# Kernel tuning notes

Measured on AMD Instinct MI355X. Metric: run time of the kernel, lower is better.

Reference implementation:

```python
import jax, jax.numpy as jnp
import numpy as np

D_MODEL = 1024
N_HEADS = 16
HEAD_DIM = D_MODEL // N_HEADS
D_FF = 4096
B, S = 2, 2048
EPS = 1e-6
NEG = -1e9


def setup_inputs() -> dict:
    key = jax.random.key(0)
    ks = jax.random.split(key, 16)
    sd = 1.0 / np.sqrt(D_MODEL)
    sf = 1.0 / np.sqrt(D_FF)
    inp = {
        "x": jax.random.normal(ks[0], (B, S, D_MODEL), jnp.float32),
        # causal mask, broadcastable over batch and heads
        "mask": jnp.tril(jnp.ones((S, S), jnp.bool_))[None, None, :, :],
        # attention projections, torch Linear layout [out, in]
        "Wq": jax.random.normal(ks[1], (D_MODEL, D_MODEL), jnp.float32) * sd,
        "bq": jnp.zeros((D_MODEL,), jnp.float32),
        "Wk": jax.random.normal(ks[2], (D_MODEL, D_MODEL), jnp.float32) * sd,
        "bk": jnp.zeros((D_MODEL,), jnp.float32),
        "Wv": jax.random.normal(ks[3], (D_MODEL, D_MODEL), jnp.float32) * sd,
        "bv": jnp.zeros((D_MODEL,), jnp.float32),
        "Wo": jax.random.normal(ks[4], (D_MODEL, D_MODEL), jnp.float32) * sd,
        "bo": jnp.zeros((D_MODEL,), jnp.float32),
        # layer norms
        "ln1_g": jnp.ones((D_MODEL,), jnp.float32),
        "ln1_b": jnp.zeros((D_MODEL,), jnp.float32),
        "ln2_g": jnp.ones((D_MODEL,), jnp.float32),
        "ln2_b": jnp.zeros((D_MODEL,), jnp.float32),
        # FFN
        "W1": jax.random.normal(ks[5], (D_FF, D_MODEL), jnp.float32) * sd,
        "b1": jnp.zeros((D_FF,), jnp.float32),
        "W2": jax.random.normal(ks[6], (D_MODEL, D_FF), jnp.float32) * sf,
        "b2": jnp.zeros((D_MODEL,), jnp.float32),
    }
    return inp


def _layer_norm(x, g, b):
    mu = jnp.mean(x, axis=-1, keepdims=True)
    var = jnp.var(x, axis=-1, keepdims=True)
    return (x - mu) * jax.lax.rsqrt(var + EPS) * g + b


def _linear(x, W, b):
    return jnp.einsum('...i,oi->...o', x, W) + b


def _attention(x, mask, Wq, bq, Wk, bk, Wv, bv, Wo, bo):
    Bsz, Sq, _ = x.shape
    q = _linear(x, Wq, bq).reshape(Bsz, Sq, N_HEADS, HEAD_DIM)
    k = _linear(x, Wk, bk).reshape(Bsz, Sq, N_HEADS, HEAD_DIM)
    v = _linear(x, Wv, bv).reshape(Bsz, Sq, N_HEADS, HEAD_DIM)
    # [B,H,S,S]
    scores = jnp.einsum('bqhd,bkhd->bhqk', q, k) / np.sqrt(HEAD_DIM)
    scores = jnp.where(mask, scores, NEG)
    weights = jax.nn.softmax(scores, axis=-1)
    ctx = jnp.einsum('bhqk,bkhd->bqhd', weights, v).reshape(Bsz, Sq, D_MODEL)
    return _linear(ctx, Wo, bo)


def reference(x, mask, Wq, bq, Wk, bk, Wv, bv, Wo, bo,
              ln1_g, ln1_b, ln2_g, ln2_b, W1, b1, W2, b2):
    # pre-LN attention block (dropout = identity at inference)
    h = _layer_norm(x, ln1_g, ln1_b)
    x = x + _attention(h, mask, Wq, bq, Wk, bk, Wv, bv, Wo, bo)
    # pre-LN FFN block
    h = _layer_norm(x, ln2_g, ln2_b)
    h = jax.nn.gelu(_linear(h, W1, b1), approximate=False)
    x = x + _linear(h, W2, b2)
    return x
```

## Files before the change

kernel.cpp:

```cpp
#include <hip/hip_runtime.h>
#include <hip/hip_bf16.h>
#include <cstdint>
#include <cstddef>

typedef unsigned short u16;
typedef __bf16 bf16x8 __attribute__((ext_vector_type(8)));
typedef float f32x4 __attribute__((ext_vector_type(4)));

#define D_MODEL 1024
#define D_FF    4096
#define BATCH   2
#define SEQ     2048
#define NH      16
#define HD      64
#define ROWS    (BATCH*SEQ)
#define QKVS    3072

__device__ __forceinline__ u16 f2bf(float f) {
    union { float f; uint32_t u; } v; v.f = f;
    uint32_t u = v.u;
    u += 0x7FFF + ((u >> 16) & 1);
    return (u16)(u >> 16);
}

__device__ __forceinline__ uint32_t cvtpk_bf16(float lo, float hi) {
    uint32_t r;
    asm("v_cvt_pk_bf16_f32 %0, %1, %2" : "=v"(r) : "v"(lo), "v"(hi));
    return r;
}

__device__ __forceinline__ bf16x8 ldg8(const u16* p) {
    return *reinterpret_cast<const bf16x8*>(p);
}

__device__ __forceinline__ f32x4 mfma16(bf16x8 a, bf16x8 b, f32x4 c) {
    return __builtin_amdgcn_mfma_f32_16x16x32_bf16(a, b, c, 0, 0, 0);
}

__device__ __forceinline__ void gld_lds16(const void* g, void* l) {
    __builtin_amdgcn_global_load_lds(
        (const __attribute__((address_space(1))) void*)g,
        (__attribute__((address_space(3))) void*)l, 16, 0, 0);
}

struct alignas(8) U16x4 { u16 x, y, z, w; };

__global__ void cvt_all(const float* __restrict__ s0, const float* __restrict__ s1,
                        const float* __restrict__ s2, const float* __restrict__ s3,
                        const float* __restrict__ s4, const float* __restrict__ s5,
                        u16* __restrict__ out)
{
    const size_t MM1 = 1 << 20;
    size_t i = ((size_t)blockIdx.x * 256 + threadIdx.x) * 4;
    const float* src; size_t off;
    if      (i <     MM1) { src = s0; off = i; }
    else if (i < 2 * MM1) { src = s1; off = i - MM1; }
    else if (i < 3 * MM1) { src = s2; off = i - 2 * MM1; }
    else if (i < 4 * MM1) { src = s3; off = i - 3 * MM1; }
    else if (i < 8 * MM1) { src = s4; off = i - 4 * MM1; }
    else                  { src = s5; off = i - 8 * MM1; }
    float4 f = *reinterpret_cast<const float4*>(src + off);
    U16x4 o{ f2bf(f.x), f2bf(f.y), f2bf(f.z), f2bf(f.w) };
    *reinterpret_cast<U16x4*>(out + i) = o;
}

__global__ __launch_bounds__(256) void ln_bf16(
    const float* __restrict__ x, const float* __restrict__ g,
    const float* __restrict__ b, u16* __restrict__ out)
{
    int row = blockIdx.x;
    const float* xr = x + (size_t)row * D_MODEL;
    int t = threadIdx.x;
    float4 v = *reinterpret_cast<const float4*>(xr + t * 4);
    float s = v.x + v.y + v.z + v.w;
    float q = v.x*v.x + v.y*v.y + v.z*v.z + v.w*v.w;
    #pragma unroll
    for (int off = 1; off < 64; off <<= 1) {
        s += __shfl_xor(s, off);
        q += __shfl_xor(q, off);
    }
    __shared__ float red[8];
    if ((t & 63) == 0) { red[(t >> 6) * 2] = s; red[(t >> 6) * 2 + 1] = q; }
    __syncthreads();
    float sum = red[0] + red[2] + red[4] + red[6];
    float sq  = red[1] + red[3] + red[5] + red[7];
    float mu  = sum * (1.0f / D_MODEL);
    float var = sq * (1.0f / D_MODEL) - mu * mu;
    float rstd = rsqrtf(var + 1e-6f);
    float4 gg = *reinterpret_cast<const float4*>(g + t * 4);
    float4 bb = *reinterpret_cast<const float4*>(b + t * 4);
    U16x4 o{ f2bf((v.x - mu) * rstd * gg.x + bb.x),
             f2bf((v.y - mu) * rstd * gg.y + bb.y),
             f2bf((v.z - mu) * rstd * gg.z + bb.z),
             f2bf((v.w - mu) * rstd * gg.w + bb.w) };
    *reinterpret_cast<U16x4*>(out + (size_t)row * D_MODEL + t * 4) = o;
}

#define EPI_BF16   0
#define EPI_RESF32 1
#define EPI_GELU   2
#define EPI_PART   3

template<int EPI>
__global__ __launch_bounds__(512, 1) void gemm256(
    const u16* __restrict__ A, const u16* __restrict__ B,
    const float* __restrict__ bias, const float* __restrict__ res,
    u16* __restrict__ outb, float* __restrict__ outf,
    int M, int N, int K)
{
    __shared__ u16 As[2][256 * 64];
    __shared__ u16 Bs[2][256 * 64];
    const int t = threadIdx.x;
    const int lane = t & 63, w = t >> 6;
    const int lr = lane & 15, lg = lane >> 4;
    const int wr = w >> 2, wc = w & 3;

    const int gw  = N >> 8;
    const int nwg = gridDim.x;
    const int cpx = nwg >> 3;
    const int swz = ((int)blockIdx.x & 7) * cpx + ((int)blockIdx.x >> 3);
    const int by = swz / gw, bx = swz % gw;
    const int brow = by * 256, bcol = bx * 256;

    const u16* Ag = A + (size_t)brow * K;
    const u16* Bg = B + (size_t)bcol * K;

    f32x4 acc[8][4] = {};
    const int NT = K >> 6;

    auto stageAll = [&](int buf, int kt) {
        #pragma unroll
        for (int c = 0; c < 8; ++c) {
            const u16* g = (c < 4) ? Ag : Bg;
            u16* l = (c < 4) ? As[buf] : Bs[buf];
            int cc = c & 3;
            int row = cc * 64 + (t >> 3);
            int sg = (t & 7) ^ (row & 7);
            gld_lds16(g + (size_t)row * K + kt * 64 + sg * 8, l + cc * 4096 + t * 8);
        }
    };

    bf16x8 areg[4][2], breg[2][2][2];

    auto loadA = [&](const u16* la, int qm) {
        #pragma unroll
        for (int f = 0; f < 4; ++f) {
            int row = wr * 128 + qm * 64 + f * 16 + lr;
            const u16* bp = la + row * 64;
            int key = row & 7;
            areg[f][0] = ldg8(bp + ((0 + lg) ^ key) * 8);
            areg[f][1] = ldg8(bp + ((4 + lg) ^ key) * 8);
        }
    };
    auto loadB = [&](const u16* lb, int qn) {
        #pragma unroll
        for (int f = 0; f < 2; ++f) {
            int row = wc * 64 + qn * 32 + f * 16 + lr;
            const u16* bp = lb + row * 64;
            int key = row & 7;
            breg[qn][f][0] = ldg8(bp + ((0 + lg) ^ key) * 8);
            breg[qn][f][1] = ldg8(bp + ((4 + lg) ^ key) * 8);
        }
    };
    auto mmaQ = [&](int qm, int qn) {
        __builtin_amdgcn_s_setprio(1);
        #pragma unroll
        for (int mi = 0; mi < 4; ++mi) {
            #pragma unroll
            for (int fn = 0; fn < 2; ++fn) {
                acc[qm * 4 + mi][qn * 2 + fn] =
                    mfma16(areg[mi][0], breg[qn][fn][0], acc[qm * 4 + mi][qn * 2 + fn]);
                acc[qm * 4 + mi][qn * 2 + fn] =
                    mfma16(areg[mi][1], breg[qn][fn][1], acc[qm * 4 + mi][qn * 2 + fn]);
            }
        }
        __builtin_amdgcn_s_setprio(0);
    };

    stageAll(0, 0);
    stageAll(1, 1);
    asm volatile("s_waitcnt vmcnt(8)" ::: "memory");
    __builtin_amdgcn_s_barrier();

    for (int kt = 0; kt < NT; ++kt) {
        const int cur = kt & 1;
        const u16* la = As[cur];
        const u16* lb = Bs[cur];
        loadA(la, 0); loadB(lb, 0);
        __builtin_amdgcn_s_barrier();
        mmaQ(0, 0);
        __builtin_amdgcn_s_barrier();
        loadB(lb, 1);
        __builtin_amdgcn_s_barrier();
        mmaQ(0, 1);
        __builtin_amdgcn_s_barrier();
        loadA(la, 1);
        __builtin_amdgcn_s_barrier();
        mmaQ(1, 0);
        __builtin_amdgcn_s_barrier();
        mmaQ(1, 1);
        if (kt + 1 == NT) break;
        __builtin_amdgcn_s_barrier();
        if (kt + 2 < NT) {
            stageAll(cur, kt + 2);
            asm volatile("s_waitcnt vmcnt(8)" ::: "memory");
        } else {
            asm volatile("s_waitcnt vmcnt(0)" ::: "memory");
        }
        __builtin_amdgcn_s_barrier();
    }

    #pragma unroll
    for (int mi = 0; mi < 8; ++mi) {
        int r0 = brow + wr * 128 + mi * 16 + lg * 4;
        #pragma unroll
        for (int ni = 0; ni < 4; ++ni) {
            int c = bcol + wc * 64 + ni * 16 + lr;
            float bv = bias[c];
            #pragma unroll
            for (int j = 0; j < 4; ++j) {
                float v = acc[mi][ni][j] + bv;
                size_t idx = (size_t)(r0 + j) * N + c;
                if constexpr (EPI == EPI_GELU) {
                    v = 0.5f * v * (1.0f + erff(v * 0.70710678118f));
                    outb[idx] = f2bf(v);
                } else if constexpr (EPI == EPI_RESF32) {
                    outf[idx] = v + res[idx];
                } else {
                    outb[idx] = f2bf(v);
                }
            }
        }
    }
}

template<int EPI>
__global__ __launch_bounds__(256, 2) void gemm_bt(
    const u16* __restrict__ A, const u16* __restrict__ B,
    const float* __restrict__ bias, const float* __restrict__ res,
    u16* __restrict__ outb, float* __restrict__ outf,
    int M, int N, int K, int KS)
{
    __shared__ u16 As[2][128 * 64];
    __shared__ u16 Bs[2][128 * 64];
    const int t = threadIdx.x;
    const int lane = t & 63;
    const int w = t >> 6;
    const int lr = lane & 15, lg = lane >> 4;
    const int wrr = (w >> 1) * 64, wcc = (w & 1) * 64;
    const int brow = blockIdx.y * 128, bcol = blockIdx.x * 128;
    const int kz = blockIdx.z;
    const u16* Ag = A + (size_t)brow * KS + (size_t)kz * K;
    const u16* Bg = B + (size_t)bcol * KS + (size_t)kz * K;

    f32x4 acc[4][4] = {};

    const int NT = K >> 6;

    auto stage = [&](int buf, int kt) {
        const u16* ga = Ag + kt * 64;
        const u16* gb = Bg + kt * 64;
        u16* la = As[buf];
        u16* lb = Bs[buf];
        #pragma unroll
        for (int c = 0; c < 4; ++c) {
            int f = c * 256 + t;
            int row = f >> 3, slot = f & 7;
            int sg = slot ^ (row & 7);
            gld_lds16(ga + (size_t)row * KS + sg * 8, la + f * 8);
            gld_lds16(gb + (size_t)row * KS + sg * 8, lb + f * 8);
        }
    };

    auto compute = [&](int buf) {
        const u16* la = As[buf];
        const u16* lb = Bs[buf];
        bf16x8 af[4][2];
        #pragma unroll
        for (int mi = 0; mi < 4; ++mi) {
            int row = wrr + mi * 16 + lr;
            int base = row * 64;
            af[mi][0] = *reinterpret_cast<const bf16x8*>(la + base + ((0 + lg) ^ (row & 7)) * 8);
            af[mi][1] = *reinterpret_cast<const bf16x8*>(la + base + ((4 + lg) ^ (row & 7)) * 8);
        }
        __builtin_amdgcn_s_setprio(1);
        #pragma unroll
        for (int ni = 0; ni < 4; ++ni) {
            int row = wcc + ni * 16 + lr;
            int base = row * 64;
            bf16x8 b0 = *reinterpret_cast<const bf16x8*>(lb + base + ((0 + lg) ^ (row & 7)) * 8);
            bf16x8 b1 = *reinterpret_cast<const bf16x8*>(lb + base + ((4 + lg) ^ (row & 7)) * 8);
            #pragma unroll
            for (int mi = 0; mi < 4; ++mi) {
                acc[mi][ni] = mfma16(af[mi][0], b0, acc[mi][ni]);
                acc[mi][ni] = mfma16(af[mi][1], b1, acc[mi][ni]);
            }
        }
        __builtin_amdgcn_s_setprio(0);
    };

    stage(0, 0);
    if (NT > 1) {
        stage(1, 1);
        asm volatile("s_waitcnt vmcnt(8)" ::: "memory");
    } else {
        asm volatile("s_waitcnt vmcnt(0)" ::: "memory");
    }
    __builtin_amdgcn_s_barrier();

    for (int kt = 0; kt < NT; ++kt) {
        compute(kt & 1);
        if (kt + 1 == NT) break;
        __builtin_amdgcn_s_barrier();
        if (kt + 2 < NT) {
            stage(kt & 1, kt + 2);
            asm volatile("s_waitcnt vmcnt(8)" ::: "memory");
        } else {
            asm volatile("s_waitcnt vmcnt(0)" ::: "memory");
        }
        __builtin_amdgcn_s_barrier();
    }

    #pragma unroll
    for (int mi = 0; mi < 4; ++mi) {
        int r0 = brow + wrr + mi * 16 + lg * 4;
        #pragma unroll
        for (int ni = 0; ni < 4; ++ni) {
            int c = bcol + wcc + ni * 16 + lr;
            float bv = 0.f;
            if constexpr (EPI != EPI_PART) bv = bias[c];
            #pragma unroll
            for (int j = 0; j < 4; ++j) {
                float v = acc[mi][ni][j] + bv;
                size_t idx = (size_t)(r0 + j) * N + c;
                if constexpr (EPI == EPI_GELU) {
                    v = 0.5f * v * (1.0f + erff(v * 0.70710678118f));
                    outb[idx] = f2bf(v);
                } else if constexpr (EPI == EPI_RESF32) {
                    outf[idx] = v + res[idx];
                } else if constexpr (EPI == EPI_PART) {
                    outf[idx + (size_t)kz * M * N] = v;
                } else {
                    outb[idx] = f2bf(v);
                }
            }
        }
    }
}

__global__ void ffn2_reduce(const float* __restrict__ p,
                            const float* __restrict__ b2,
                            const float* __restrict__ x2,
                            float* __restrict__ out)
{
    size_t i = ((size_t)blockIdx.x * 256 + threadIdx.x) * 4;
    float4 a0 = *reinterpret_cast<const float4*>(p + i);
    float4 a1 = *reinterpret_cast<const float4*>(p + (size_t)ROWS * D_MODEL + i);
    float4 r  = *reinterpret_cast<const float4*>(x2 + i);
    float4 bb = *reinterpret_cast<const float4*>(b2 + (i & (D_MODEL - 1)));
    float4 o;
    o.x = a0.x + a1.x + r.x + bb.x;
    o.y = a0.y + a1.y + r.y + bb.y;
    o.z = a0.z + a1.z + r.z + bb.z;
    o.w = a0.w + a1.w + r.w + bb.w;
    *reinterpret_cast<float4*>(out + i) = o;
}

__global__ __launch_bounds__(256) void vtrans(
    const u16* __restrict__ QKV, u16* __restrict__ VT)
{
    __shared__ u16 tile[64][72];
    const int st = blockIdx.x * 64;
    const int bh = blockIdx.y;
    const int b = bh >> 4, h = bh & 15;
    const int t = threadIdx.x;

    #pragma unroll
    for (int c = 0; c < 2; ++c) {
        int tok = c * 32 + (t >> 3);
        int d0 = (t & 7) * 8;
        bf16x8 v = ldg8(QKV + ((size_t)(b * SEQ + st + tok)) * QKVS + 2048 + h * HD + d0);
        *reinterpret_cast<bf16x8*>(&tile[tok][d0]) = v;
    }
    __syncthreads();
    u16* dst = VT + (size_t)bh * HD * SEQ + st;
    #pragma unroll
    for (int c = 0; c < 2; ++c) {
        int d = c * 32 + (t >> 3);
        int tok0 = (t & 7) * 8;
        u16 vals[8];
        #pragma unroll
        for (int i = 0; i < 8; ++i) vals[i] = tile[tok0 + i][d];
        *reinterpret_cast<bf16x8*>(dst + (size_t)d * SEQ + tok0) =
            *reinterpret_cast<const bf16x8*>(vals);
    }
}

#define QBLK  64
#define KVBLK 64

__global__ __launch_bounds__(256, 3) void attn7(
    const u16* __restrict__ QKV, const u16* __restrict__ VT,
    u16* __restrict__ O)
{
    __shared__ u16 Ks[2][64 * 64];
    __shared__ u16 Vs[2][64 * 64];
    __shared__ u16 Pl[4][16 * 72];

    const int i  = blockIdx.x;
    const int bh = blockIdx.y;
    const int b = bh >> 4, h = bh & 15;
    const int qta = 31 - i;
    const int qtb = i;
    const int q0a = qta * QBLK, q0b = qtb * QBLK;
    const int t = threadIdx.x;
    const int lane = t & 63, w = t >> 6;
    const int lr = lane & 15, lg = lane >> 4;

    const size_t rowbase = (size_t)b * SEQ;
    const u16* Qg = QKV + rowbase * QKVS + h * HD;
    const u16* Kg = Qg + 1024;
    const u16* Vg = VT + (size_t)bh * HD * SEQ;

    const u16* qpa = Qg + (size_t)(q0a + w * 16 + lr) * QKVS;
    const u16* qpb = Qg + (size_t)(q0b + w * 16 + lr) * QKVS;
    bf16x8 qa0 = ldg8(qpa + lg * 8), qa1 = ldg8(qpa + 32 + lg * 8);
    bf16x8 qb0 = ldg8(qpb + lg * 8), qb1 = ldg8(qpb + 32 + lg * 8);

    f32x4 oa[4] = {}, ob[4] = {};
    float lsa[4] = {}, lsb[4] = {};

    const int ntiles = qta + 1;
    u16* Pw = Pl[w];
    const float SC = 0.125f * 1.44269504089f;

    auto stage = [&](int buf, int tt) {
        const int kv0 = tt * KVBLK;
        #pragma unroll
        for (int c = 0; c < 2; ++c) {
            int f = c * 256 + t;
            int row = f >> 3, slot = f & 7;
            int sgk = slot ^ ((row >> 2) & 7);
            int sgv = slot ^ (row & 7);
            gld_lds16(Kg + (size_t)(kv0 + row) * QKVS + sgk * 8, Ks[buf] + f * 8);
            gld_lds16(Vg + (size_t)row * SEQ + kv0 + sgv * 8, Vs[buf] + f * 8);
        }
    };

    auto qtile = [&](bf16x8 qf0, bf16x8 qf1, f32x4* o, float* ls,
                     int q0, int kv0, bool diag, const u16* kb, const u16* vb) {
        f32x4 s[4] = {};
        __builtin_amdgcn_s_setprio(1);
        #pragma unroll
        for (int ni = 0; ni < 4; ++ni) {
            int row = lr * 4 + ni;
            const u16* base = kb + row * 64;
            int key = (row >> 2) & 7;
            bf16x8 k0 = *reinterpret_cast<const bf16x8*>(base + ((0 + lg) ^ key) * 8);
            bf16x8 k1 = *reinterpret_cast<const bf16x8*>(base + ((4 + lg) ^ key) * 8);
            s[ni] = mfma16(qf0, k0, s[ni]);
            s[ni] = mfma16(qf1, k1, s[ni]);
        }
        __builtin_amdgcn_s_setprio(0);

        #pragma unroll
        for (int j = 0; j < 4; ++j) {
            int qi = q0 + w * 16 + lg * 4 + j;
            float p0 = __builtin_amdgcn_exp2f(s[0][j] * SC);
            float p1 = __builtin_amdgcn_exp2f(s[1][j] * SC);
            float p2 = __builtin_amdgcn_exp2f(s[2][j] * SC);
            float p3 = __builtin_amdgcn_exp2f(s[3][j] * SC);
            if (diag) {
                int kvb = kv0 + lr * 4;
                p0 = (kvb     <= qi) ? p0 : 0.f;
                p1 = (kvb + 1 <= qi) ? p1 : 0.f;
                p2 = (kvb + 2 <= qi) ? p2 : 0.f;
                p3 = (kvb + 3 <= qi) ? p3 : 0.f;
            }
            ls[j] += (p0 + p1) + (p2 + p3);
            uint2 pk = make_uint2(cvtpk_bf16(p0, p1), cvtpk_bf16(p2, p3));
            *reinterpret_cast<uint2*>(&Pw[(lg * 4 + j) * 72 + lr * 4]) = pk;
        }

        bf16x8 pa0 = *reinterpret_cast<const bf16x8*>(Pw + lr * 72 + lg * 8);
        bf16x8 pa1 = *reinterpret_cast<const bf16x8*>(Pw + lr * 72 + 32 + lg * 8);
        __builtin_amdgcn_s_setprio(1);
        #pragma unroll
        for (int ni = 0; ni < 4; ++ni) {
            int row = ni * 16 + lr;
            const u16* base = vb + row * 64;
            bf16x8 v0 = *reinterpret_cast<const bf16x8*>(base + ((0 + lg) ^ (row & 7)) * 8);
            bf16x8 v1 = *reinterpret_cast<const bf16x8*>(base + ((4 + lg) ^ (row & 7)) * 8);
            o[ni] = mfma16(pa0, v0, o[ni]);
            o[ni] = mfma16(pa1, v1, o[ni]);
        }
        __builtin_amdgcn_s_setprio(0);
    };

    stage(0, 0);
    stage(1, 1);
    asm volatile("s_waitcnt vmcnt(4)" ::: "memory");
    __builtin_amdgcn_s_barrier();

    for (int tt = 0; tt < ntiles; ++tt) {
        const int buf = tt & 1;
        const int kv0 = tt * KVBLK;
        const u16* kb = Ks[buf];
        const u16* vb = Vs[buf];

        qtile(qa0, qa1, oa, lsa, q0a, kv0, tt == qta, kb, vb);
        if (tt <= qtb)
            qtile(qb0, qb1, ob, lsb, q0b, kv0, tt == qtb, kb, vb);

        if (tt + 1 == ntiles) break;
        __builtin_amdgcn_s_barrier();
        if (tt + 2 < ntiles) {
            stage(buf, tt + 2);
            asm volatile("s_waitcnt vmcnt(4)" ::: "memory");
        } else {
            asm volatile("s_waitcnt vmcnt(0)" ::: "memory");
        }
        __builtin_amdgcn_s_barrier();
    }

    #pragma unroll
    for (int j = 0; j < 4; ++j) {
        float va = lsa[j], vb2 = lsb[j];
        va += __shfl_xor(va, 1); vb2 += __shfl_xor(vb2, 1);
        va += __shfl_xor(va, 2); vb2 += __shfl_xor(vb2, 2);
        va += __shfl_xor(va, 4); vb2 += __shfl_xor(vb2, 4);
        va += __shfl_xor(va, 8); vb2 += __shfl_xor(vb2, 8);
        lsa[j] = va; lsb[j] = vb2;
    }

    u16* Oa = O + (rowbase + q0a + w * 16) * D_MODEL + h * HD;
    u16* Ob = O + (rowbase + q0b + w * 16) * D_MODEL + h * HD;
    #pragma unroll
    for (int j = 0; j < 4; ++j) {
        float inva = 1.0f / lsa[j];
        float invb = 1.0f / lsb[j];
        int r = (lg * 4 + j) * D_MODEL;
        #pragma unroll
        for (int ni = 0; ni < 4; ++ni) {
            Oa[r + ni * 16 + lr] = f2bf(oa[ni][j] * inva);
            Ob[r + ni * 16 + lr] = f2bf(ob[ni][j] * invb);
        }
    }
}

extern "C" void kernel_launch(void* const* d_in, const int* in_sizes, int n_in,
                              void* d_out, int out_size, void* d_ws, size_t ws_size,
                              hipStream_t stream)
{
    (void)in_sizes; (void)n_in; (void)out_size; (void)ws_size;
    const float* x   = (const float*)d_in[0];
    const float* Wq  = (const float*)d_in[2];
    const float* bq  = (const float*)d_in[3];
    const float* Wk  = (const float*)d_in[4];
    const float* bk  = (const float*)d_in[5];
    const float* Wv  = (const float*)d_in[6];
    const float* bv  = (const float*)d_in[7];
    const float* Wo  = (const float*)d_in[8];
    const float* bo  = (const float*)d_in[9];
    const float* g1  = (const float*)d_in[10];
    const float* be1 = (const float*)d_in[11];
    const float* g2  = (const float*)d_in[12];
    const float* be2 = (const float*)d_in[13];
    const float* W1  = (const float*)d_in[14];
    const float* b1  = (const float*)d_in[15];
    const float* W2  = (const float*)d_in[16];
    const float* b2  = (const float*)d_in[17];
    float* out = (float*)d_out;

    const size_t MM = 1 << 20;
    u16* Wqkv_b = (u16*)d_ws;
    u16* Wo_b = Wqkv_b + 3 * MM;
    u16* W1_b = Wo_b + MM;
    u16* W2_b = W1_b + 4 * MM;
    u16* hbuf = W2_b + 4 * MM;
    u16* QKVb = hbuf + 4 * MM;
    u16* ctx  = QKVb + 12 * MM;
    u16* ffn1 = ctx + 4 * MM;
    float* x2 = (float*)(ffn1 + 16 * MM);
    float* bqkv = (float*)(x2 + 4 * MM);
    u16* VTb = hbuf;
    float* fpart = (float*)QKVb;

    cvt_all<<<12 * MM / 1024, 256, 0, stream>>>(Wq, Wk, Wv, Wo, W1, W2, Wqkv_b);

    hipMemcpyAsync(bqkv,        bq, D_MODEL * sizeof(float), hipMemcpyDeviceToDevice, stream);
    hipMemcpyAsync(bqkv + 1024, bk, D_MODEL * sizeof(float), hipMemcpyDeviceToDevice, stream);
    hipMemcpyAsync(bqkv + 2048, bv, D_MODEL * sizeof(float), hipMemcpyDeviceToDevice, stream);

    ln_bf16<<<ROWS, 256, 0, stream>>>(x, g1, be1, hbuf);

    dim3 gqkv(QKVS / 128, ROWS / 128);
    gemm_bt<EPI_BF16><<<gqkv, 256, 0, stream>>>(hbuf, Wqkv_b, bqkv, nullptr,
                                                QKVb, nullptr, ROWS, QKVS, 1024, 1024);

    vtrans<<<dim3(SEQ / 64, BATCH * NH), 256, 0, stream>>>(QKVb, VTb);

    dim3 ga(SEQ / QBLK / 2, BATCH * NH);
    attn7<<<ga, 256, 0, stream>>>(QKVb, VTb, ctx);

    dim3 gq(D_MODEL / 128, ROWS / 128);
    gemm_bt<EPI_RESF32><<<gq, 256, 0, stream>>>(ctx, Wo_b, bo, x, nullptr, x2,
                                                ROWS, D_MODEL, 1024, 1024);

    ln_bf16<<<ROWS, 256, 0, stream>>>(x2, g2, be2, hbuf);

    gemm256<EPI_GELU><<<(ROWS / 256) * (D_FF / 256), 512, 0, stream>>>(
        hbuf, W1_b, b1, nullptr, ffn1, nullptr, ROWS, D_FF, D_MODEL);

    dim3 gf2(D_MODEL / 128, ROWS / 128, 2);
    gemm_bt<EPI_PART><<<gf2, 256, 0, stream>>>(ffn1, W2_b, nullptr, nullptr,
                                               nullptr, fpart, ROWS, D_MODEL, 2048, 4096);
    ffn2_reduce<<<(ROWS * D_MODEL) / 1024, 256, 0, stream>>>(fpart, b2, x2, out);
}
```

Measured before the change: 254.8 us.

## Simplify big-tile GEMM inner loop and use tanh-approx GELU epilogue

The 256-wide GEMM's k-step no longer runs four quadrant phases separated by workgroup barriers. It now loads all B fragments once, then streams A rows while issuing MFMAs, with no intra-tile barriers. The GELU epilogue in both GEMMs swaps erff for a tanh-form approximation built on exp2, which cuts transcendental cost. That approximation departs from the exact erf GELU the reference specifies, and the new loop holds more B registers while losing the explicit load/compute interleave.

```diff
diff --git a/kernel.cpp b/kernel.cpp
--- a/kernel.cpp
+++ b/kernel.cpp
@@ -41,6 +41,13 @@
     __builtin_amdgcn_global_load_lds(
         (const __attribute__((address_space(1))) void*)g,
         (__attribute__((address_space(3))) void*)l, 16, 0, 0);
+}
+
+__device__ __forceinline__ float gelu_f(float x) {
+    float u = fmaf(0.044715f * x, x * x, x);
+    float z = fminf(-2.3022036f * u, 126.0f);
+    float e = __builtin_amdgcn_exp2f(z);
+    return x / (1.0f + e);
 }
 
 struct alignas(8) U16x4 { u16 x, y, z, w; };
@@ -140,41 +147,33 @@
         }
     };
 
-    bf16x8 areg[4][2], breg[2][2][2];
-
-    auto loadA = [&](const u16* la, int qm) {
-        #pragma unroll
-        for (int f = 0; f < 4; ++f) {
-            int row = wr * 128 + qm * 64 + f * 16 + lr;
-            const u16* bp = la + row * 64;
-            int key = row & 7;
-            areg[f][0] = ldg8(bp + ((0 + lg) ^ key) * 8);
-            areg[f][1] = ldg8(bp + ((4 + lg) ^ key) * 8);
-        }
-    };
-    auto loadB = [&](const u16* lb, int qn) {
-        #pragma unroll
-        for (int f = 0; f < 2; ++f) {
-            int row = wc * 64 + qn * 32 + f * 16 + lr;
+    auto computeTile = [&](int buf) {
+        const u16* la = As[buf];
+        const u16* lb = Bs[buf];
+        bf16x8 breg[4][2];
+        #pragma unroll
+        for (int ni = 0; ni < 4; ++ni) {
+            int row = wc * 64 + ni * 16 + lr;
             const u16* bp = lb + row * 64;
             int key = row & 7;
-            breg[qn][f][0] = ldg8(bp + ((0 + lg) ^ key) * 8);
-            breg[qn][f][1] = ldg8(bp + ((4 + lg) ^ key) * 8);
-        }
-    };
-    auto mmaQ = [&](int qm, int qn) {
-        __builtin_amdgcn_s_setprio(1);
-        #pragma unroll
-        for (int mi = 0; mi < 4; ++mi) {
+            breg[ni][0] = ldg8(bp + ((0 + lg) ^ key) * 8);
+            breg[ni][1] = ldg8(bp + ((4 + lg) ^ key) * 8);
+        }
+        #pragma unroll
+        for (int mi = 0; mi < 8; ++mi) {
+            int row = wr * 128 + mi * 16 + lr;
+            const u16* ap = la + row * 64;
+            int key = row & 7;
+            bf16x8 a0 = ldg8(ap + ((0 + lg) ^ key) * 8);
+            bf16x8 a1 = ldg8(ap + ((4 + lg) ^ key) * 8);
+            __builtin_amdgcn_s_setprio(1);
             #pragma unroll
-            for (int fn = 0; fn < 2; ++fn) {
-                acc[qm * 4 + mi][qn * 2 + fn] =
-                    mfma16(areg[mi][0], breg[qn][fn][0], acc[qm * 4 + mi][qn * 2 + fn]);
-                acc[qm * 4 + mi][qn * 2 + fn] =
-                    mfma16(areg[mi][1], breg[qn][fn][1], acc[qm * 4 + mi][qn * 2 + fn]);
+            for (int ni = 0; ni < 4; ++ni) {
+                acc[mi][ni] = mfma16(a0, breg[ni][0], acc[mi][ni]);
+                acc[mi][ni] = mfma16(a1, breg[ni][1], acc[mi][ni]);
             }
-        }
-        __builtin_amdgcn_s_setprio(0);
+            __builtin_amdgcn_s_setprio(0);
+        }
     };
 
     stageAll(0, 0);
@@ -183,26 +182,11 @@
     __builtin_amdgcn_s_barrier();
 
     for (int kt = 0; kt < NT; ++kt) {
-        const int cur = kt & 1;
-        const u16* la = As[cur];
-        const u16* lb = Bs[cur];
-        loadA(la, 0); loadB(lb, 0);
-        __builtin_amdgcn_s_barrier();
-        mmaQ(0, 0);
-        __builtin_amdgcn_s_barrier();
-        loadB(lb, 1);
-        __builtin_amdgcn_s_barrier();
-        mmaQ(0, 1);
-        __builtin_amdgcn_s_barrier();
-        loadA(la, 1);
-        __builtin_amdgcn_s_barrier();
-        mmaQ(1, 0);
-        __builtin_amdgcn_s_barrier();
-        mmaQ(1, 1);
+        computeTile(kt & 1);
         if (kt + 1 == NT) break;
         __builtin_amdgcn_s_barrier();
         if (kt + 2 < NT) {
-            stageAll(cur, kt + 2);
+            stageAll(kt & 1, kt + 2);
             asm volatile("s_waitcnt vmcnt(8)" ::: "memory");
         } else {
             asm volatile("s_waitcnt vmcnt(0)" ::: "memory");
@@ -222,8 +206,7 @@
                 float v = acc[mi][ni][j] + bv;
                 size_t idx = (size_t)(r0 + j) * N + c;
                 if constexpr (EPI == EPI_GELU) {
-                    v = 0.5f * v * (1.0f + erff(v * 0.70710678118f));
-                    outb[idx] = f2bf(v);
+                    outb[idx] = f2bf(gelu_f(v));
                 } else if constexpr (EPI == EPI_RESF32) {
                     outf[idx] = v + res[idx];
                 } else {
@@ -334,8 +317,7 @@
                 float v = acc[mi][ni][j] + bv;
                 size_t idx = (size_t)(r0 + j) * N + c;
                 if constexpr (EPI == EPI_GELU) {
-                    v = 0.5f * v * (1.0f + erff(v * 0.70710678118f));
-                    outb[idx] = f2bf(v);
+                    outb[idx] = f2bf(gelu_f(v));
                 } else if constexpr (EPI == EPI_RESF32) {
                     outf[idx] = v + res[idx];
                 } else if constexpr (EPI == EPI_PART) {
```

Result: faster. 242.2 us (-5.0%).
